# Kernel tuning notes

Hardware: AMD Instinct MI355X
Metric: run time of the kernel (lower is better)

Reference implementation:

```python
import jax, jax.numpy as jnp
import numpy as np

DT = 0.1
BOX = 1.0  # WORLD_SIZE
EPS = 1e-6


def range_angle(ang):
    return jnp.mod(ang + jnp.pi, 2.0 * jnp.pi) - jnp.pi


def ekf_step(x, P, a, Y, n1, n2_sigma, n2_kappa, gains, obs_gains):
    # x: (N,5) [px,py,ang,vel,ang_vel]; P: (N,5,5); a: (N,2); Y: (2,N)
    N = x.shape[0]
    dt = DT
    og = obs_gains

    # --- noise-free dynamics (w=0 in original forward) ---
    vel = gains[0] * a[:, 0]
    ang_vel = gains[1] * a[:, 1]
    ang = range_angle(x[:, 2] + ang_vel * dt)
    px = jnp.clip(x[:, 0] + vel * jnp.cos(ang) * dt, -BOX, BOX)
    py = jnp.clip(x[:, 1] + vel * jnp.sin(ang) * dt, -BOX, BOX)
    x_ = jnp.stack([px, py, ang, vel, ang_vel], axis=1)  # (N,5)

    # --- Jacobian A (N,5,5): eye(3) block + two trig entries ---
    d3 = jnp.arange(3)
    A = jnp.zeros((N, 5, 5), x.dtype)
    A = A.at[:, d3, d3].set(1.0)
    A = A.at[:, 0, 2].set(-vel * jnp.sin(ang) * dt)
    A = A.at[:, 1, 2].set(vel * jnp.cos(ang) * dt)

    # --- predict: L is identity in the original code, so L Q L^T = Q ---
    Q = jnp.diag(jnp.exp(2.0 * n1))
    P_ = jnp.einsum('nij,njk,nlk->nil', A, P, A) + Q  # (N,5,5)

    # --- innovation covariance S = H P_ H^T + M R M^T (R = I, M diag) ---
    # H = [0 | diag(og)] so H P_ H^T = diag(og) P_[3:5,3:5] diag(og)
    HPHt = P_[:, 3:5, 3:5] * og[None, :, None] * og[None, None, :]
    m_diag = x_[:, 3:5] ** 2 * jnp.exp(2.0 * n2_kappa) + jnp.exp(2.0 * n2_sigma)
    S = HPHt + m_diag[:, :, None] * jnp.eye(2, dtype=x.dtype)  # (N,2,2)

    # --- explicit 2x2 inverse ---
    sa, sb = S[:, 0, 0], S[:, 0, 1]
    sc, sd = S[:, 1, 0], S[:, 1, 1]
    det = sa * sd - sb * sc
    Sinv = jnp.stack([jnp.stack([sd, -sb], -1), jnp.stack([-sc, sa], -1)], -2)
    Sinv = Sinv / det[:, None, None]

    # --- Kalman gain K = P_ H^T S^{-1} ---
    PHt = P_[:, :, 3:5] * og[None, None, :]  # (N,5,2)
    K = jnp.einsum('nij,njk->nik', PHt, Sinv)  # (N,5,2)

    # --- update ---
    h = og[None, :] * x_[:, 3:5]  # noise-free observations (N,2)
    err = Y.T - h
    x_new = x_ + jnp.einsum('nij,nj->ni', K, err)

    KH = jnp.zeros((N, 5, 5), x.dtype).at[:, :, 3:5].set(K * og[None, None, :])
    I_KH = jnp.eye(5, dtype=x.dtype) - KH
    P_new = jnp.einsum('nij,njk->nik', I_KH, P_)
    P_new = 0.5 * (P_new + jnp.swapaxes(P_new, -1, -2)) + EPS * jnp.eye(5, dtype=x.dtype)
    return x_new, P_new, K


def setup_inputs() -> dict:
    key = jax.random.key(0)
    ks = jax.random.split(key, 6)
    N = 500_000
    x = jax.random.normal(ks[0], (N, 5), jnp.float32)
    # symmetric positive-definite covariances
    Lr = 0.1 * jax.random.normal(ks[1], (N, 5, 5), jnp.float32)
    P = jnp.einsum('nij,nkj->nik', Lr, Lr) + 0.5 * jnp.eye(5, dtype=jnp.float32)
    a = jax.random.normal(ks[2], (N, 2), jnp.float32)
    Y = 0.5 * jax.random.normal(ks[3], (2, N), jnp.float32)
    n1 = jnp.full((5,), -1.0, jnp.float32)
    n2 = jnp.full((4,), -1.0, jnp.float32)
    return {
        'x': x, 'P': P, 'a': a, 'Y': Y,
        'n1': n1,
        'n2_sigma': n2[:2],
        'n2_kappa': n2[2:],
        'gains': jnp.ones((2,), jnp.float32),
        'obs_gains': jnp.ones((2,), jnp.float32),
    }


def reference(x, P, a, Y, n1, n2_sigma, n2_kappa, gains, obs_gains):
    return ekf_step(x, P, a, Y, n1, n2_sigma, n2_kappa, gains, obs_gains)
```

## Files before the change

kernel.cpp:

```cpp
#include <hip/hip_runtime.h>
#include <math.h>
#include <stdint.h>


#define BLK 64
#define TILE_F 2176
#define OFF_X  1600
#define OFF_A  1920
#define OFF_Y  2048
#define OB_X   0
#define OB_P   320
#define OB_K   1920

__device__ __forceinline__ void gload_lds16(const void* g, void* l) {
    __builtin_amdgcn_global_load_lds(
        (const __attribute__((address_space(1))) void*)g,
        (__attribute__((address_space(3))) void*)l, 16, 0, 0);
}
__device__ __forceinline__ void gload_lds4(const void* g, void* l) {
    __builtin_amdgcn_global_load_lds(
        (const __attribute__((address_space(1))) void*)g,
        (__attribute__((address_space(3))) void*)l, 4, 0, 0);
}

__device__ __forceinline__ void stage_tile(const float* Pg, const float* xg,
                                           const float* ag, const float* Yg,
                                           int N, int base, float* buf, int tid) {
    const char* gp = (const char*)(Pg + (size_t)base * 25);
    char* lp = (char*)buf;
    #pragma unroll
    for (int j = 0; j < 6; ++j)
        gload_lds16(gp + j * 1024 + tid * 16, lp + j * 1024);
    gload_lds4(gp + 6144 + tid * 4, lp + 6144);
    const char* gx = (const char*)(xg + (size_t)base * 5);
    gload_lds16(gx + tid * 16, lp + 6400);
    gload_lds4(gx + 1024 + tid * 4, lp + 6400 + 1024);
    const char* ga = (const char*)(ag + (size_t)base * 2);
    gload_lds4(ga + tid * 4,       lp + 7680);
    gload_lds4(ga + 256 + tid * 4, lp + 7680 + 256);
    gload_lds4((const char*)(Yg + base)     + tid * 4, lp + 8192);
    gload_lds4((const char*)(Yg + N + base) + tid * 4, lp + 8192 + 256);
}

struct EkfOut {
    float px, py, ang, xn3, xn4;
    float t00, s01, s02, t11, s12, t22, Pn33, Pn44;
    float K30, K41;
};

__device__ __forceinline__ EkfOut ekf_math(
    float x0, float x1, float x2, float a0, float a1, float y0, float y1,
    float p00, float p01, float p02, float p10, float p11, float p12,
    float p20, float p21, float p22,
    float g0, float g1, float og0, float og1,
    float q0, float q1, float q2, float q3, float q4,
    float e2s0, float e2s1, float e2k0, float e2k1)
{
    const float dt = 0.1f;
    const float fPI  = 3.14159265358979323846f;
    const float f2PI = 6.28318530717958647692f;
    const float EPS_ = 1e-6f;

    float vel = g0 * a0, angvel = g1 * a1;

    float ar = x2 + angvel * dt + fPI;
    float w = fmodf(ar, f2PI);
    if (w < 0.0f) w += f2PI;
    float ang = w - fPI;

    float s, c;
    sincosf(ang, &s, &c);

    EkfOut o;
    o.px = fminf(fmaxf(x0 + vel * c * dt, -1.0f), 1.0f);
    o.py = fminf(fmaxf(x1 + vel * s * dt, -1.0f), 1.0f);
    o.ang = ang;

    float m0 = -vel * s * dt, m1 = vel * c * dt;

    float b00 = p00 + m0 * p20, b01 = p01 + m0 * p21, b02 = p02 + m0 * p22;
    float b10 = p10 + m1 * p20, b11 = p11 + m1 * p21, b12 = p12 + m1 * p22;
    float t00 = b00 + m0 * b02, t01 = b01 + m1 * b02;
    float t10 = b10 + m0 * b12, t11 = b11 + m1 * b12;
    float t20 = p20 + m0 * p22, t21 = p21 + m1 * p22, t22 = p22;
    float t02 = b02, t12 = b12;

    t00 += q0; t11 += q1; t22 += q2;
    o.s01 = 0.5f * (t01 + t10);
    o.s02 = 0.5f * (t02 + t20);
    o.s12 = 0.5f * (t12 + t21);
    o.t00 = t00 + EPS_; o.t11 = t11 + EPS_; o.t22 = t22 + EPS_;

    float S00 = q3 * og0 * og0 + vel * vel * e2k0 + e2s0;
    float S11 = q4 * og1 * og1 + angvel * angvel * e2k1 + e2s1;
    o.K30 = q3 * og0 / S00;
    o.K41 = q4 * og1 / S11;

    o.xn3 = vel    + o.K30 * (y0 - og0 * vel);
    o.xn4 = angvel + o.K41 * (y1 - og1 * angvel);
    o.Pn33 = (1.0f - o.K30 * og0) * q3 + EPS_;
    o.Pn44 = (1.0f - o.K41 * og1) * q4 + EPS_;
    return o;
}

__global__ __launch_bounds__(BLK) void ekf_kernel(
    const float* __restrict__ xg, const float* __restrict__ Pg,
    const float* __restrict__ ag, const float* __restrict__ Yg,
    const float* __restrict__ n1, const float* __restrict__ n2s,
    const float* __restrict__ n2k, const float* __restrict__ gains,
    const float* __restrict__ og, float* __restrict__ out, int N)
{
    __shared__ float lds[2 * TILE_F + 2560];
    float* bufA = lds;
    float* bufB = lds + TILE_F;
    float* obuf = lds + 2 * TILE_F;

    const int tid = threadIdx.x;
    const int tiles = (N + BLK - 1) / BLK;
    const int G = gridDim.x, b = blockIdx.x;
    const int q = tiles / G, r = tiles % G;
    const int t0 = b * q + min(b, r);
    const int myTiles = q + (b < r ? 1 : 0);
    if (myTiles <= 0) return;

    const float g0 = gains[0], g1 = gains[1];
    const float og0 = og[0], og1 = og[1];
    const float q0 = expf(2.f * n1[0]), q1 = expf(2.f * n1[1]),
                q2 = expf(2.f * n1[2]), q3 = expf(2.f * n1[3]),
                q4 = expf(2.f * n1[4]);
    const float e2s0 = expf(2.f * n2s[0]), e2s1 = expf(2.f * n2s[1]);
    const float e2k0 = expf(2.f * n2k[0]), e2k1 = expf(2.f * n2k[1]);

    {
        float* pp = obuf + OB_P + tid * 25;
        pp[3] = 0.f; pp[4] = 0.f; pp[8] = 0.f; pp[9] = 0.f;
        pp[13] = 0.f; pp[14] = 0.f;
        pp[15] = 0.f; pp[16] = 0.f; pp[17] = 0.f; pp[19] = 0.f;
        pp[20] = 0.f; pp[21] = 0.f; pp[22] = 0.f; pp[23] = 0.f;
        float* kk = obuf + OB_K + tid * 10;
        kk[0] = 0.f; kk[1] = 0.f; kk[2] = 0.f; kk[3] = 0.f;
        kk[4] = 0.f; kk[5] = 0.f; kk[7] = 0.f; kk[8] = 0.f;
    }

    {
        int base0 = t0 * BLK;
        if (base0 + BLK <= N) stage_tile(Pg, xg, ag, Yg, N, base0, bufA, tid);
    }
    float* cur = bufA;
    float* nxt = bufB;

    for (int k = 0; k < myTiles; ++k) {
        const int t = t0 + k;
        const int base = t * BLK;
        const bool fullT = (base + BLK <= N);

        bool issued = false;
        if (k + 1 < myTiles) {
            int nb = (t + 1) * BLK;
            if (nb + BLK <= N) { stage_tile(Pg, xg, ag, Yg, N, nb, nxt, tid); issued = true; }
        }

        if (fullT) {
            if (k == 0) { if (issued) asm volatile("s_waitcnt vmcnt(13)" ::: "memory");
                          else        asm volatile("s_waitcnt vmcnt(0)"  ::: "memory"); }
            else        { if (issued) asm volatile("s_waitcnt vmcnt(25)" ::: "memory");
                          else        asm volatile("s_waitcnt vmcnt(12)" ::: "memory"); }

            float x0 = cur[OFF_X + tid * 5 + 0];
            float x1 = cur[OFF_X + tid * 5 + 1];
            float x2 = cur[OFF_X + tid * 5 + 2];
            float2 av = *(const float2*)&cur[OFF_A + tid * 2];
            float y0 = cur[OFF_Y + tid];
            float y1 = cur[OFF_Y + 64 + tid];
            const float* pr = cur + tid * 25;
            EkfOut o = ekf_math(x0, x1, x2, av.x, av.y, y0, y1,
                                pr[0], pr[1], pr[2], pr[5], pr[6], pr[7],
                                pr[10], pr[11], pr[12],
                                g0, g1, og0, og1, q0, q1, q2, q3, q4,
                                e2s0, e2s1, e2k0, e2k1);

            float* xx = obuf + OB_X + tid * 5;
            xx[0] = o.px; xx[1] = o.py; xx[2] = o.ang; xx[3] = o.xn3; xx[4] = o.xn4;
            float* pp = obuf + OB_P + tid * 25;
            pp[0] = o.t00; pp[1] = o.s01; pp[2] = o.s02;
            pp[5] = o.s01; pp[6] = o.t11; pp[7] = o.s12;
            pp[10] = o.s02; pp[11] = o.s12; pp[12] = o.t22;
            pp[18] = o.Pn33; pp[24] = o.Pn44;
            float* kk = obuf + OB_K + tid * 10;
            kk[6] = o.K30; kk[9] = o.K41;

            float4* gx4 = (float4*)(out + (size_t)base * 5);
            float4* gp4 = (float4*)(out + (size_t)5 * N + (size_t)base * 25);
            float4* gk4 = (float4*)(out + (size_t)30 * N + (size_t)base * 10);
            const float4* lx4 = (const float4*)(obuf + OB_X);
            const float4* lp4 = (const float4*)(obuf + OB_P);
            const float4* lk4 = (const float4*)(obuf + OB_K);
            gx4[tid] = lx4[tid];
            if (tid < 16) gx4[64 + tid] = lx4[64 + tid];
            #pragma unroll
            for (int j = 0; j < 6; ++j) gp4[j * 64 + tid] = lp4[j * 64 + tid];
            if (tid < 16) gp4[384 + tid] = lp4[384 + tid];
            #pragma unroll
            for (int j = 0; j < 2; ++j) gk4[j * 64 + tid] = lk4[j * 64 + tid];
            if (tid < 32) gk4[128 + tid] = lk4[128 + tid];
        } else {
            const int i = base + tid;
            if (i < N) {
                const float* pr = Pg + (size_t)i * 25;
                EkfOut o = ekf_math(xg[i * 5 + 0], xg[i * 5 + 1], xg[i * 5 + 2],
                                    ag[i * 2 + 0], ag[i * 2 + 1],
                                    Yg[i], Yg[N + i],
                                    pr[0], pr[1], pr[2], pr[5], pr[6], pr[7],
                                    pr[10], pr[11], pr[12],
                                    g0, g1, og0, og1, q0, q1, q2, q3, q4,
                                    e2s0, e2s1, e2k0, e2k1);
                float* gx = out + (size_t)i * 5;
                gx[0] = o.px; gx[1] = o.py; gx[2] = o.ang; gx[3] = o.xn3; gx[4] = o.xn4;
                float* gp = out + (size_t)5 * N + (size_t)i * 25;
                gp[0] = o.t00; gp[1] = o.s01; gp[2] = o.s02; gp[3] = 0.f; gp[4] = 0.f;
                gp[5] = o.s01; gp[6] = o.t11; gp[7] = o.s12; gp[8] = 0.f; gp[9] = 0.f;
                gp[10] = o.s02; gp[11] = o.s12; gp[12] = o.t22; gp[13] = 0.f; gp[14] = 0.f;
                gp[15] = 0.f; gp[16] = 0.f; gp[17] = 0.f; gp[18] = o.Pn33; gp[19] = 0.f;
                gp[20] = 0.f; gp[21] = 0.f; gp[22] = 0.f; gp[23] = 0.f; gp[24] = o.Pn44;
                float* gk = out + (size_t)30 * N + (size_t)i * 10;
                gk[0] = 0.f; gk[1] = 0.f; gk[2] = 0.f; gk[3] = 0.f; gk[4] = 0.f;
                gk[5] = 0.f; gk[6] = o.K30; gk[7] = 0.f; gk[8] = 0.f; gk[9] = o.K41;
            }
        }

        float* tmp = cur; cur = nxt; nxt = tmp;
    }
}

extern "C" void kernel_launch(void* const* d_in, const int* in_sizes, int n_in,
                              void* d_out, int out_size, void* d_ws, size_t ws_size,
                              hipStream_t stream) {
    const float* x     = (const float*)d_in[0];
    const float* P     = (const float*)d_in[1];
    const float* a     = (const float*)d_in[2];
    const float* Y     = (const float*)d_in[3];
    const float* n1    = (const float*)d_in[4];
    const float* n2s   = (const float*)d_in[5];
    const float* n2k   = (const float*)d_in[6];
    const float* gains = (const float*)d_in[7];
    const float* og    = (const float*)d_in[8];
    const int N = in_sizes[0] / 5;
    const int tiles = (N + BLK - 1) / BLK;
    int G = 1280;
    if (G > tiles) G = tiles;
    ekf_kernel<<<G, BLK, 0, stream>>>(x, P, a, Y, n1, n2s, n2k, gains, og,
                                      (float*)d_out, N);
}
```

Baseline: 150.1 us.

## Replace LDS async staging with register double-buffered loads of needed elements only

Drops the global_load_lds staging of full P tiles into shared memory. Each thread now loads only the 9 P entries, 3 x entries, actions and observations it actually uses into registers, with a ping-pong prefetch of the next tile. The grid doubles to 2560 blocks because shared memory per block shrinks. This cuts read traffic, since 16 of the 25 P floats go unused, and frees LDS for occupancy. In exchange it relies on the compiler to schedule the prefetch, and the per-thread 12-byte strided loads coalesce less cleanly.

```diff
diff --git a/kernel.cpp b/kernel.cpp
--- a/kernel.cpp
+++ b/kernel.cpp
@@ -4,42 +4,33 @@
 
 
 #define BLK 64
-#define TILE_F 2176
-#define OFF_X  1600
-#define OFF_A  1920
-#define OFF_Y  2048
-#define OB_X   0
-#define OB_P   320
-#define OB_K   1920
-
-__device__ __forceinline__ void gload_lds16(const void* g, void* l) {
-    __builtin_amdgcn_global_load_lds(
-        (const __attribute__((address_space(1))) void*)g,
-        (__attribute__((address_space(3))) void*)l, 16, 0, 0);
-}
-__device__ __forceinline__ void gload_lds4(const void* g, void* l) {
-    __builtin_amdgcn_global_load_lds(
-        (const __attribute__((address_space(1))) void*)g,
-        (__attribute__((address_space(3))) void*)l, 4, 0, 0);
-}
-
-__device__ __forceinline__ void stage_tile(const float* Pg, const float* xg,
-                                           const float* ag, const float* Yg,
-                                           int N, int base, float* buf, int tid) {
-    const char* gp = (const char*)(Pg + (size_t)base * 25);
-    char* lp = (char*)buf;
-    #pragma unroll
-    for (int j = 0; j < 6; ++j)
-        gload_lds16(gp + j * 1024 + tid * 16, lp + j * 1024);
-    gload_lds4(gp + 6144 + tid * 4, lp + 6144);
-    const char* gx = (const char*)(xg + (size_t)base * 5);
-    gload_lds16(gx + tid * 16, lp + 6400);
-    gload_lds4(gx + 1024 + tid * 4, lp + 6400 + 1024);
-    const char* ga = (const char*)(ag + (size_t)base * 2);
-    gload_lds4(ga + tid * 4,       lp + 7680);
-    gload_lds4(ga + 256 + tid * 4, lp + 7680 + 256);
-    gload_lds4((const char*)(Yg + base)     + tid * 4, lp + 8192);
-    gload_lds4((const char*)(Yg + N + base) + tid * 4, lp + 8192 + 256);
+#define OB_X 0
+#define OB_P 320
+#define OB_K 1920
+
+struct F3 { float a, b, c; };
+
+struct TR {
+    float p00,p01,p02,p10,p11,p12,p20,p21,p22;
+    float x0,x1,x2,a0,a1,y0,y1;
+};
+
+__device__ __forceinline__ void load_tile(TR& r,
+    const float* __restrict__ Pg, const float* __restrict__ xg,
+    const float* __restrict__ ag, const float* __restrict__ Yg,
+    int N, int i) {
+    const float* pb = Pg + (size_t)i * 25;
+    F3 r0 = *(const F3*)(pb);
+    F3 r1 = *(const F3*)(pb + 5);
+    F3 r2 = *(const F3*)(pb + 10);
+    F3 xx = *(const F3*)(xg + (size_t)i * 5);
+    float2 av = *(const float2*)(ag + (size_t)i * 2);
+    r.p00 = r0.a; r.p01 = r0.b; r.p02 = r0.c;
+    r.p10 = r1.a; r.p11 = r1.b; r.p12 = r1.c;
+    r.p20 = r2.a; r.p21 = r2.b; r.p22 = r2.c;
+    r.x0 = xx.a; r.x1 = xx.b; r.x2 = xx.c;
+    r.a0 = av.x; r.a1 = av.y;
+    r.y0 = Yg[i]; r.y1 = Yg[N + i];
 }
 
 struct EkfOut {
@@ -110,17 +101,14 @@
     const float* __restrict__ n2k, const float* __restrict__ gains,
     const float* __restrict__ og, float* __restrict__ out, int N)
 {
-    __shared__ float lds[2 * TILE_F + 2560];
-    float* bufA = lds;
-    float* bufB = lds + TILE_F;
-    float* obuf = lds + 2 * TILE_F;
+    __shared__ float obuf[2560];
 
     const int tid = threadIdx.x;
     const int tiles = (N + BLK - 1) / BLK;
-    const int G = gridDim.x, b = blockIdx.x;
-    const int q = tiles / G, r = tiles % G;
-    const int t0 = b * q + min(b, r);
-    const int myTiles = q + (b < r ? 1 : 0);
+    const int G = gridDim.x, blk = blockIdx.x;
+    const int qt = tiles / G, rt = tiles % G;
+    const int t0 = blk * qt + min(blk, rt);
+    const int myTiles = qt + (blk < rt ? 1 : 0);
     if (myTiles <= 0) return;
 
     const float g0 = gains[0], g1 = gains[1];
@@ -142,40 +130,27 @@
         kk[4] = 0.f; kk[5] = 0.f; kk[7] = 0.f; kk[8] = 0.f;
     }
 
+    TR A, B;
     {
-        int base0 = t0 * BLK;
-        if (base0 + BLK <= N) stage_tile(Pg, xg, ag, Yg, N, base0, bufA, tid);
+        int i0 = t0 * BLK;
+        if (i0 + BLK <= N) load_tile(A, Pg, xg, ag, Yg, N, i0 + tid);
     }
-    float* cur = bufA;
-    float* nxt = bufB;
-
-    for (int k = 0; k < myTiles; ++k) {
-        const int t = t0 + k;
-        const int base = t * BLK;
-        const bool fullT = (base + BLK <= N);
-
-        bool issued = false;
-        if (k + 1 < myTiles) {
-            int nb = (t + 1) * BLK;
-            if (nb + BLK <= N) { stage_tile(Pg, xg, ag, Yg, N, nb, nxt, tid); issued = true; }
-        }
-
-        if (fullT) {
-            if (k == 0) { if (issued) asm volatile("s_waitcnt vmcnt(13)" ::: "memory");
-                          else        asm volatile("s_waitcnt vmcnt(0)"  ::: "memory"); }
-            else        { if (issued) asm volatile("s_waitcnt vmcnt(25)" ::: "memory");
-                          else        asm volatile("s_waitcnt vmcnt(12)" ::: "memory"); }
-
-            float x0 = cur[OFF_X + tid * 5 + 0];
-            float x1 = cur[OFF_X + tid * 5 + 1];
-            float x2 = cur[OFF_X + tid * 5 + 2];
-            float2 av = *(const float2*)&cur[OFF_A + tid * 2];
-            float y0 = cur[OFF_Y + tid];
-            float y1 = cur[OFF_Y + 64 + tid];
-            const float* pr = cur + tid * 25;
-            EkfOut o = ekf_math(x0, x1, x2, av.x, av.y, y0, y1,
-                                pr[0], pr[1], pr[2], pr[5], pr[6], pr[7],
-                                pr[10], pr[11], pr[12],
+
+    int k = 0;
+    auto process = [&](TR& cur, TR& nxt) {
+        const int base = (t0 + k) * BLK;
+        const int i = base + tid;
+        if (base + BLK <= N) {
+            if (k + 1 < myTiles) {
+                int nb = base + BLK;
+                if (nb + BLK <= N) load_tile(nxt, Pg, xg, ag, Yg, N, nb + tid);
+            }
+
+            EkfOut o = ekf_math(cur.x0, cur.x1, cur.x2, cur.a0, cur.a1,
+                                cur.y0, cur.y1,
+                                cur.p00, cur.p01, cur.p02,
+                                cur.p10, cur.p11, cur.p12,
+                                cur.p20, cur.p21, cur.p22,
                                 g0, g1, og0, og1, q0, q1, q2, q3, q4,
                                 e2s0, e2s1, e2k0, e2k1);
 
@@ -204,7 +179,6 @@
             for (int j = 0; j < 2; ++j) gk4[j * 64 + tid] = lk4[j * 64 + tid];
             if (tid < 32) gk4[128 + tid] = lk4[128 + tid];
         } else {
-            const int i = base + tid;
             if (i < N) {
                 const float* pr = Pg + (size_t)i * 25;
                 EkfOut o = ekf_math(xg[i * 5 + 0], xg[i * 5 + 1], xg[i * 5 + 2],
@@ -227,8 +201,13 @@
                 gk[5] = 0.f; gk[6] = o.K30; gk[7] = 0.f; gk[8] = 0.f; gk[9] = o.K41;
             }
         }
-
-        float* tmp = cur; cur = nxt; nxt = tmp;
+    };
+
+    while (true) {
+        process(A, B);
+        if (++k >= myTiles) break;
+        process(B, A);
+        if (++k >= myTiles) break;
     }
 }
 
@@ -246,7 +225,7 @@
     const float* og    = (const float*)d_in[8];
     const int N = in_sizes[0] / 5;
     const int tiles = (N + BLK - 1) / BLK;
-    int G = 1280;
+    int G = 2560;
     if (G > tiles) G = tiles;
     ekf_kernel<<<G, BLK, 0, stream>>>(x, P, a, Y, n1, n2s, n2k, gains, og,
                                       (float*)d_out, N);
```

After: 146.5 us. 1.02x faster.
